# Optimization experiments

Hardware: AMD Instinct MI355X
Metric: run time of the kernel (lower is better)

The kernel has to match this reference:

```python
import jax, jax.numpy as jnp
import numpy as np

B, S, H, D, DM = 2, 512, 8, 32, 256  # batch, seq_len, n_head, d_k, d_model


def setup_inputs() -> dict:
    key = jax.random.key(0)
    ks = jax.random.split(key, 8)
    scale = 0.02
    return {
        "hidden_states": jax.random.normal(ks[0], (B, S, DM), dtype=jnp.float32),
        "rpe": jax.random.normal(ks[1], (B, S, S, D), dtype=jnp.float32),
        "w_q": jax.random.normal(ks[2], (DM, H * D), dtype=jnp.float32) * scale,
        "w_k": jax.random.normal(ks[3], (DM, H * D), dtype=jnp.float32) * scale,
        "w_v": jax.random.normal(ks[4], (DM, H * D), dtype=jnp.float32) * scale,
        "fc_w": jax.random.normal(ks[5], (H * D, DM), dtype=jnp.float32) * scale,
        "fc_b": jnp.zeros((DM,), dtype=jnp.float32),
        "ln_w": jnp.ones((DM,), dtype=jnp.float32),
        "ln_b": jnp.zeros((DM,), dtype=jnp.float32),
        "station_num": 256,
    }


def reference(hidden_states, rpe, w_q, w_k, w_v, fc_w, fc_b, ln_w, ln_b, station_num):
    b, s, dm = hidden_states.shape
    d = rpe.shape[-1]
    h = w_q.shape[1] // d

    def heads(x, w):
        # (b, s, dm) @ (dm, h*d) -> (b, h, s, d)
        return (x @ w).reshape(b, s, h, d).transpose(0, 2, 1, 3)

    q = heads(hidden_states, w_q)
    k = heads(hidden_states, w_k)
    v = heads(hidden_states, w_v)

    # torch: (q.unsqueeze(2) * k.unsqueeze(3) * rpe.unsqueeze(1)).sum(-1)
    # scores[b,h,i,j] = sum_d q[b,h,j,d] * k[b,h,i,d] * rpe[b,i,j,d]
    scores = jnp.einsum('bhjd,bhid,bijd->bhij', q, k, rpe) / jnp.sqrt(jnp.float32(d))

    # shielded mask: column j visible if j < station_num, plus the diagonal
    col = jnp.arange(s) < station_num                  # (s,)
    mask = col[None, :] | jnp.eye(s, dtype=bool)        # (s, s)
    scores = jnp.where(mask[None, None], scores, jnp.float32(-1e10))

    attn = jax.nn.softmax(scores, axis=-1)              # (b, h, s, s)
    out = jnp.einsum('bhij,bhjd->bhid', attn, v)        # (b, h, s, d)
    out = out.transpose(0, 2, 1, 3).reshape(b, s, h * d)

    ctx = out @ fc_w + fc_b + hidden_states             # residual
    mu = jnp.mean(ctx, axis=-1, keepdims=True)
    var = jnp.mean(jnp.square(ctx - mu), axis=-1, keepdims=True)
    ctx = (ctx - mu) / jnp.sqrt(var + 1e-6) * ln_w + ln_b
    return ctx
```

## Files before the change

### kernel.cpp

```cpp
#include <hip/hip_runtime.h>
#include <hip/hip_bf16.h>

#define B_  2
#define S_  512
#define H_  8
#define D_  32
#define DM_ 256
#define HD_ 256
#define NROW 4
#define TI  8
#define HC  2
#define NR  (TI * HC)
#define PSTR 520

__global__ __launch_bounds__(256) void qkv_kernel(
    const float* __restrict__ hid, const float* __restrict__ wq,
    const float* __restrict__ wk, const float* __restrict__ wv,
    float* __restrict__ qo, float* __restrict__ ko, float* __restrict__ vo)
{
  __shared__ float hs[NROW][DM_];
  const int r0 = blockIdx.x * NROW;
  const float* w   = (blockIdx.y == 0) ? wq : (blockIdx.y == 1) ? wk : wv;
  float*       out = (blockIdx.y == 0) ? qo : (blockIdx.y == 1) ? ko : vo;
  const int tid = threadIdx.x;

  for (int idx = tid; idx < NROW * DM_; idx += 256)
    hs[idx >> 8][idx & 255] = hid[r0 * DM_ + idx];
  __syncthreads();

  float acc[NROW] = {0.f, 0.f, 0.f, 0.f};
  const float* wp = w + tid;
  #pragma unroll 8
  for (int c4 = 0; c4 < DM_ / 4; ++c4) {
    const float w0 = wp[(4 * c4 + 0) * HD_];
    const float w1 = wp[(4 * c4 + 1) * HD_];
    const float w2 = wp[(4 * c4 + 2) * HD_];
    const float w3 = wp[(4 * c4 + 3) * HD_];
    #pragma unroll
    for (int r = 0; r < NROW; ++r) {
      const float4 hv = reinterpret_cast<const float4*>(&hs[r][0])[c4];
      acc[r] = fmaf(hv.x, w0, acc[r]);
      acc[r] = fmaf(hv.y, w1, acc[r]);
      acc[r] = fmaf(hv.z, w2, acc[r]);
      acc[r] = fmaf(hv.w, w3, acc[r]);
    }
  }
  const int h = tid >> 5, d = tid & 31;
  #pragma unroll
  for (int r = 0; r < NROW; ++r) {
    const int g = r0 + r;
    const int b = g >> 9, s = g & (S_ - 1);
    out[((b * H_ + h) * S_ + s) * D_ + d] = acc[r];
  }
}

__global__ __launch_bounds__(512, 2) void attn_kernel(
    const float* __restrict__ rpe, const float* __restrict__ q_ws,
    const float* __restrict__ k_ws, const float* __restrict__ v_ws,
    const int* __restrict__ station_p, float* __restrict__ o_ws)
{
  __shared__ float k_lds[NR * D_];
  __shared__ float p_lds[NR][PSTR];
  __shared__ float sums[NR];
  __shared__ float4 redv[8][NR][8];

  const int tid = threadIdx.x;
  const int n   = blockIdx.x;
  const int hg  = (n >> 3) & 3;
  const int t   = (n & 7) | ((n >> 5) << 3);
  const int b   = t >> 6;
  const int i0  = (t & 63) * TI;
  const int h0  = hg * HC;

  int station = station_p[0];
  if (station > S_) station = S_;
  if (station < 0)  station = 0;

  {
    const int r = tid >> 5, d = tid & 31;
    const int hh = r >> 3, ii = r & 7;
    k_lds[tid] = k_ws[((b * H_ + h0 + hh) * S_ + i0 + ii) * D_ + d];
  }
  __syncthreads();

  const int j = tid;
  const bool jlt = (j < station);
  const bool intile = (j >= i0) && (j < i0 + TI);

  float4 q0[8], q1[8];
  if (jlt || intile) {
    const float4* qp0 = reinterpret_cast<const float4*>(
        q_ws + ((b * H_ + h0 + 0) * S_ + j) * D_);
    const float4* qp1 = reinterpret_cast<const float4*>(
        q_ws + ((b * H_ + h0 + 1) * S_ + j) * D_);
    #pragma unroll
    for (int tt = 0; tt < 8; ++tt) { q0[tt] = qp0[tt]; q1[tt] = qp1[tt]; }
  }

  const float4* rbase = reinterpret_cast<const float4*>(
      rpe + (((size_t)b * S_ + i0) * S_ + j) * D_);
  const int rstride = S_ * D_ / 4;

  #pragma unroll
  for (int ii = 0; ii < TI; ++ii) {
    const int i = i0 + ii;
    const bool ok = jlt || (j == i);
    float s0 = -1e30f, s1 = -1e30f;
    if (ok) {
      const float4* rp  = rbase + ii * rstride;
      const float4* kp0 = reinterpret_cast<const float4*>(&k_lds[(0 * TI + ii) * D_]);
      const float4* kp1 = reinterpret_cast<const float4*>(&k_lds[(1 * TI + ii) * D_]);
      float a0 = 0.f, a1 = 0.f;
      #pragma unroll
      for (int tt = 0; tt < 8; ++tt) {
        const float4 rv = rp[tt];
        const float4 k0 = kp0[tt];
        const float4 k1 = kp1[tt];
        a0 = fmaf(q0[tt].x * k0.x, rv.x, a0);
        a0 = fmaf(q0[tt].y * k0.y, rv.y, a0);
        a0 = fmaf(q0[tt].z * k0.z, rv.z, a0);
        a0 = fmaf(q0[tt].w * k0.w, rv.w, a0);
        a1 = fmaf(q1[tt].x * k1.x, rv.x, a1);
        a1 = fmaf(q1[tt].y * k1.y, rv.y, a1);
        a1 = fmaf(q1[tt].z * k1.z, rv.z, a1);
        a1 = fmaf(q1[tt].w * k1.w, rv.w, a1);
      }
      s0 = a0 * 0.17677669529663687f;
      s1 = a1 * 0.17677669529663687f;
    }
    p_lds[0 * TI + ii][j] = s0;
    p_lds[1 * TI + ii][j] = s1;
  }
  __syncthreads();

  {
    const int w = tid >> 6, lane = tid & 63;
    for (int rr = w; rr < NR; rr += 8) {
      float m = -1e30f;
      #pragma unroll
      for (int jj = lane; jj < S_; jj += 64) m = fmaxf(m, p_lds[rr][jj]);
      #pragma unroll
      for (int o = 32; o; o >>= 1) m = fmaxf(m, __shfl_xor(m, o, 64));
      float sum = 0.f;
      #pragma unroll
      for (int jj = lane; jj < S_; jj += 64) {
        const float p = __expf(p_lds[rr][jj] - m);
        p_lds[rr][jj] = p;
        sum += p;
      }
      #pragma unroll
      for (int o = 32; o; o >>= 1) sum += __shfl_xor(sum, o, 64);
      if (lane == 0) sums[rr] = sum;
    }
  }
  __syncthreads();

  {
    const int part = tid >> 6;
    const int lane = tid & 63;
    const int ii = lane >> 3, d4 = lane & 7;
    const float4* vp0 = reinterpret_cast<const float4*>(
        v_ws + ((size_t)(b * H_ + h0 + 0) * S_) * D_) + d4;
    const float4* vp1 = reinterpret_cast<const float4*>(
        v_ws + ((size_t)(b * H_ + h0 + 1) * S_) * D_) + d4;
    float4 a0 = {0.f, 0.f, 0.f, 0.f};
    float4 a1 = {0.f, 0.f, 0.f, 0.f};
    #pragma unroll 4
    for (int jj = part; jj < station; jj += 8) {
      const float p0 = p_lds[0 * TI + ii][jj];
      const float p1 = p_lds[1 * TI + ii][jj];
      const float4 v0 = vp0[jj * (D_ / 4)];
      const float4 v1 = vp1[jj * (D_ / 4)];
      a0.x = fmaf(p0, v0.x, a0.x); a0.y = fmaf(p0, v0.y, a0.y);
      a0.z = fmaf(p0, v0.z, a0.z); a0.w = fmaf(p0, v0.w, a0.w);
      a1.x = fmaf(p1, v1.x, a1.x); a1.y = fmaf(p1, v1.y, a1.y);
      a1.z = fmaf(p1, v1.z, a1.z); a1.w = fmaf(p1, v1.w, a1.w);
    }
    const int ig = i0 + ii;
    if (ig >= station && part == (ig & 7)) {
      const float p0 = p_lds[0 * TI + ii][ig];
      const float p1 = p_lds[1 * TI + ii][ig];
      const float4 v0 = vp0[ig * (D_ / 4)];
      const float4 v1 = vp1[ig * (D_ / 4)];
      a0.x = fmaf(p0, v0.x, a0.x); a0.y = fmaf(p0, v0.y, a0.y);
      a0.z = fmaf(p0, v0.z, a0.z); a0.w = fmaf(p0, v0.w, a0.w);
      a1.x = fmaf(p1, v1.x, a1.x); a1.y = fmaf(p1, v1.y, a1.y);
      a1.z = fmaf(p1, v1.z, a1.z); a1.w = fmaf(p1, v1.w, a1.w);
    }
    redv[part][0 * TI + ii][d4] = a0;
    redv[part][1 * TI + ii][d4] = a1;
  }
  __syncthreads();
  if (tid < NR * 8) {
    const int r = tid >> 3, d4 = tid & 7;
    float4 a = redv[0][r][d4];
    #pragma unroll
    for (int p = 1; p < 8; ++p) {
      const float4 x = redv[p][r][d4];
      a.x += x.x; a.y += x.y; a.z += x.z; a.w += x.w;
    }
    const float inv = 1.f / sums[r];
    a.x *= inv; a.y *= inv; a.z *= inv; a.w *= inv;
    const int hh = r >> 3, ii = r & 7;
    reinterpret_cast<float4*>(
        o_ws + ((b * H_ + h0 + hh) * S_ + i0 + ii) * D_)[d4] = a;
  }
}

__global__ __launch_bounds__(256) void fc_ln_kernel(
    const float* __restrict__ o_ws, const float* __restrict__ fc_w,
    const float* __restrict__ fc_b, const float* __restrict__ hid,
    const float* __restrict__ ln_w, const float* __restrict__ ln_b,
    float* __restrict__ out)
{
  __shared__ float orow[NROW][HD_];
  __shared__ float red[NROW][4];
  const int tid = threadIdx.x;
  const int r0 = blockIdx.x * NROW;

  for (int idx = tid; idx < NROW * HD_; idx += 256) {
    const int r = idx >> 8, m = idx & 255;
    const int g = r0 + r;
    const int b = g >> 9, i = g & (S_ - 1);
    orow[r][m] = o_ws[((b * H_ + (m >> 5)) * S_ + i) * D_ + (m & 31)];
  }
  __syncthreads();

  float acc[NROW] = {0.f, 0.f, 0.f, 0.f};
  const float* wp = fc_w + tid;
  #pragma unroll 8
  for (int n4 = 0; n4 < HD_ / 4; ++n4) {
    const float w0 = wp[(4 * n4 + 0) * DM_];
    const float w1 = wp[(4 * n4 + 1) * DM_];
    const float w2 = wp[(4 * n4 + 2) * DM_];
    const float w3 = wp[(4 * n4 + 3) * DM_];
    #pragma unroll
    for (int r = 0; r < NROW; ++r) {
      const float4 ov = reinterpret_cast<const float4*>(&orow[r][0])[n4];
      acc[r] = fmaf(ov.x, w0, acc[r]);
      acc[r] = fmaf(ov.y, w1, acc[r]);
      acc[r] = fmaf(ov.z, w2, acc[r]);
      acc[r] = fmaf(ov.w, w3, acc[r]);
    }
  }
  const float bias = fc_b[tid];
  #pragma unroll
  for (int r = 0; r < NROW; ++r) acc[r] += bias + hid[(r0 + r) * DM_ + tid];

  const int w = tid >> 6, lane = tid & 63;
  float mu[NROW];
  #pragma unroll
  for (int r = 0; r < NROW; ++r) {
    float s = acc[r];
    #pragma unroll
    for (int o = 32; o; o >>= 1) s += __shfl_xor(s, o, 64);
    if (lane == 0) red[r][w] = s;
  }
  __syncthreads();
  #pragma unroll
  for (int r = 0; r < NROW; ++r)
    mu[r] = (red[r][0] + red[r][1] + red[r][2] + red[r][3]) * (1.f / DM_);
  __syncthreads();
  #pragma unroll
  for (int r = 0; r < NROW; ++r) {
    const float dd = acc[r] - mu[r];
    float s = dd * dd;
    #pragma unroll
    for (int o = 32; o; o >>= 1) s += __shfl_xor(s, o, 64);
    if (lane == 0) red[r][w] = s;
  }
  __syncthreads();
  const float lw = ln_w[tid], lb = ln_b[tid];
  #pragma unroll
  for (int r = 0; r < NROW; ++r) {
    const float var = (red[r][0] + red[r][1] + red[r][2] + red[r][3]) * (1.f / DM_);
    out[(r0 + r) * DM_ + tid] =
        (acc[r] - mu[r]) * rsqrtf(var + 1e-6f) * lw + lb;
  }
}

extern "C" void kernel_launch(void* const* d_in, const int* in_sizes, int n_in,
                              void* d_out, int out_size, void* d_ws, size_t ws_size,
                              hipStream_t stream) {
  const float* hid = (const float*)d_in[0];
  const float* rpe = (const float*)d_in[1];
  const float* wq  = (const float*)d_in[2];
  const float* wk  = (const float*)d_in[3];
  const float* wv  = (const float*)d_in[4];
  const float* fcw = (const float*)d_in[5];
  const float* fcb = (const float*)d_in[6];
  const float* lnw = (const float*)d_in[7];
  const float* lnb = (const float*)d_in[8];
  const int* station = (const int*)d_in[9];
  float* out = (float*)d_out;

  const size_t per = (size_t)B_ * H_ * S_ * D_;
  float* q_ws = (float*)d_ws;
  float* k_ws = q_ws + per;
  float* v_ws = k_ws + per;
  float* o_ws = v_ws + per;

  dim3 gA(B_ * S_ / NROW, 3);
  qkv_kernel<<<gA, 256, 0, stream>>>(hid, wq, wk, wv, q_ws, k_ws, v_ws);
  attn_kernel<<<B_ * (S_ / TI) * (H_ / HC), 512, 0, stream>>>(
      rpe, q_ws, k_ws, v_ws, station, o_ws);
  fc_ln_kernel<<<B_ * S_ / NROW, 256, 0, stream>>>(o_ws, fcw, fcb, hid, lnw, lnb, out);
}
```

Before: 168.4 us.

## Halve attention block size, loop over key halves, restrict softmax to visible columns

The attention kernel now runs 256 threads per block, and each thread handles two key columns. Each thread accumulates all 8 query rows per column in registers and reads K straight from global memory instead of staging it in LDS. The softmax only scans visible columns (j < station) plus the diagonal, instead of all 512 entries. The PV reduction splits across 4 partitions instead of 8. The aim is to cut wasted softmax work on masked columns and reuse q across rows. The cost is higher register pressure and less parallelism per block.

```diff
diff --git a/kernel.cpp b/kernel.cpp
--- a/kernel.cpp
+++ b/kernel.cpp
@@ -54,15 +54,14 @@
   }
 }
 
-__global__ __launch_bounds__(512, 2) void attn_kernel(
+__global__ __launch_bounds__(256, 3) void attn_kernel(
     const float* __restrict__ rpe, const float* __restrict__ q_ws,
     const float* __restrict__ k_ws, const float* __restrict__ v_ws,
     const int* __restrict__ station_p, float* __restrict__ o_ws)
 {
-  __shared__ float k_lds[NR * D_];
   __shared__ float p_lds[NR][PSTR];
   __shared__ float sums[NR];
-  __shared__ float4 redv[8][NR][8];
+  __shared__ float4 redv[4][NR][8];
 
   const int tid = threadIdx.x;
   const int n   = blockIdx.x;
@@ -73,84 +72,90 @@
   const int h0  = hg * HC;
 
   int station = station_p[0];
-  if (station > S_) station = S_;
-  if (station < 0)  station = 0;
-
-  {
-    const int r = tid >> 5, d = tid & 31;
-    const int hh = r >> 3, ii = r & 7;
-    k_lds[tid] = k_ws[((b * H_ + h0 + hh) * S_ + i0 + ii) * D_ + d];
-  }
-  __syncthreads();
-
-  const int j = tid;
-  const bool jlt = (j < station);
-  const bool intile = (j >= i0) && (j < i0 + TI);
-
-  float4 q0[8], q1[8];
-  if (jlt || intile) {
-    const float4* qp0 = reinterpret_cast<const float4*>(
-        q_ws + ((b * H_ + h0 + 0) * S_ + j) * D_);
-    const float4* qp1 = reinterpret_cast<const float4*>(
-        q_ws + ((b * H_ + h0 + 1) * S_ + j) * D_);
-    #pragma unroll
-    for (int tt = 0; tt < 8; ++tt) { q0[tt] = qp0[tt]; q1[tt] = qp1[tt]; }
-  }
-
-  const float4* rbase = reinterpret_cast<const float4*>(
-      rpe + (((size_t)b * S_ + i0) * S_ + j) * D_);
-  const int rstride = S_ * D_ / 4;
-
-  #pragma unroll
-  for (int ii = 0; ii < TI; ++ii) {
-    const int i = i0 + ii;
-    const bool ok = jlt || (j == i);
-    float s0 = -1e30f, s1 = -1e30f;
-    if (ok) {
-      const float4* rp  = rbase + ii * rstride;
-      const float4* kp0 = reinterpret_cast<const float4*>(&k_lds[(0 * TI + ii) * D_]);
-      const float4* kp1 = reinterpret_cast<const float4*>(&k_lds[(1 * TI + ii) * D_]);
-      float a0 = 0.f, a1 = 0.f;
+  station = station > S_ ? S_ : (station < 0 ? 0 : station);
+
+  const float* kb0 = k_ws + ((b * H_ + h0) * S_ + i0) * D_;
+  const float* kb1 = kb0 + S_ * D_;
+
+  #pragma unroll 1
+  for (int half = 0; half < 2; ++half) {
+    const int j  = tid + half * 256;
+    const int dt = j - i0;
+    const bool diag = ((unsigned)dt < (unsigned)TI);
+    if ((j < station) || diag) {
+      float a0[TI], a1[TI];
+      #pragma unroll
+      for (int ii = 0; ii < TI; ++ii) { a0[ii] = 0.f; a1[ii] = 0.f; }
+      const float* qp0 = q_ws + ((b * H_ + h0) * S_ + j) * D_;
+      const float* qp1 = qp0 + S_ * D_;
+      const float* rp  = rpe + (((size_t)b * S_ + i0) * S_ + j) * D_;
       #pragma unroll
       for (int tt = 0; tt < 8; ++tt) {
-        const float4 rv = rp[tt];
-        const float4 k0 = kp0[tt];
-        const float4 k1 = kp1[tt];
-        a0 = fmaf(q0[tt].x * k0.x, rv.x, a0);
-        a0 = fmaf(q0[tt].y * k0.y, rv.y, a0);
-        a0 = fmaf(q0[tt].z * k0.z, rv.z, a0);
-        a0 = fmaf(q0[tt].w * k0.w, rv.w, a0);
-        a1 = fmaf(q1[tt].x * k1.x, rv.x, a1);
-        a1 = fmaf(q1[tt].y * k1.y, rv.y, a1);
-        a1 = fmaf(q1[tt].z * k1.z, rv.z, a1);
-        a1 = fmaf(q1[tt].w * k1.w, rv.w, a1);
+        const float4 q0 = *reinterpret_cast<const float4*>(qp0 + tt * 4);
+        const float4 q1 = *reinterpret_cast<const float4*>(qp1 + tt * 4);
+        #pragma unroll
+        for (int ii = 0; ii < TI; ++ii) {
+          const float4 rv = *reinterpret_cast<const float4*>(rp + ii * (S_ * D_) + tt * 4);
+          const float4 k0 = *reinterpret_cast<const float4*>(kb0 + ii * D_ + tt * 4);
+          const float4 k1 = *reinterpret_cast<const float4*>(kb1 + ii * D_ + tt * 4);
+          a0[ii] = fmaf(q0.x * k0.x, rv.x, a0[ii]);
+          a0[ii] = fmaf(q0.y * k0.y, rv.y, a0[ii]);
+          a0[ii] = fmaf(q0.z * k0.z, rv.z, a0[ii]);
+          a0[ii] = fmaf(q0.w * k0.w, rv.w, a0[ii]);
+          a1[ii] = fmaf(q1.x * k1.x, rv.x, a1[ii]);
+          a1[ii] = fmaf(q1.y * k1.y, rv.y, a1[ii]);
+          a1[ii] = fmaf(q1.z * k1.z, rv.z, a1[ii]);
+          a1[ii] = fmaf(q1.w * k1.w, rv.w, a1[ii]);
+        }
       }
-      s0 = a0 * 0.17677669529663687f;
-      s1 = a1 * 0.17677669529663687f;
-    }
-    p_lds[0 * TI + ii][j] = s0;
-    p_lds[1 * TI + ii][j] = s1;
+      const float sc = 0.17677669529663687f;
+      if (j < station) {
+        #pragma unroll
+        for (int ii = 0; ii < TI; ++ii) {
+          p_lds[ii][j]      = a0[ii] * sc;
+          p_lds[TI + ii][j] = a1[ii] * sc;
+        }
+      } else {
+        #pragma unroll
+        for (int ii = 0; ii < TI; ++ii) {
+          if (dt == ii) {
+            p_lds[ii][j]      = a0[ii] * sc;
+            p_lds[TI + ii][j] = a1[ii] * sc;
+          }
+        }
+      }
+    }
   }
   __syncthreads();
 
   {
     const int w = tid >> 6, lane = tid & 63;
-    for (int rr = w; rr < NR; rr += 8) {
+    #pragma unroll
+    for (int k = 0; k < 4; ++k) {
+      const int r  = w * 4 + k;
+      const int ii = r & 7;
+      const int ig = i0 + ii;
+      const bool dx = (ig >= station);
       float m = -1e30f;
-      #pragma unroll
-      for (int jj = lane; jj < S_; jj += 64) m = fmaxf(m, p_lds[rr][jj]);
+      for (int jj = lane; jj < station; jj += 64) m = fmaxf(m, p_lds[r][jj]);
+      const float dv = dx ? p_lds[r][ig] : -1e30f;
+      m = fmaxf(m, dv);
       #pragma unroll
       for (int o = 32; o; o >>= 1) m = fmaxf(m, __shfl_xor(m, o, 64));
       float sum = 0.f;
-      #pragma unroll
-      for (int jj = lane; jj < S_; jj += 64) {
-        const float p = __expf(p_lds[rr][jj] - m);
-        p_lds[rr][jj] = p;
-        sum += p;
+      for (int jj = lane; jj < station; jj += 64) {
+        const float e = __expf(p_lds[r][jj] - m);
+        p_lds[r][jj] = e;
+        sum += e;
       }
       #pragma unroll
       for (int o = 32; o; o >>= 1) sum += __shfl_xor(sum, o, 64);
-      if (lane == 0) sums[rr] = sum;
+      if (dx) {
+        const float e = __expf(dv - m);
+        sum += e;
+        if (lane == 0) p_lds[r][ig] = e;
+      }
+      if (lane == 0) sums[r] = sum;
     }
   }
   __syncthreads();
@@ -159,43 +164,41 @@
     const int part = tid >> 6;
     const int lane = tid & 63;
     const int ii = lane >> 3, d4 = lane & 7;
-    const float4* vp0 = reinterpret_cast<const float4*>(
-        v_ws + ((size_t)(b * H_ + h0 + 0) * S_) * D_) + d4;
-    const float4* vp1 = reinterpret_cast<const float4*>(
-        v_ws + ((size_t)(b * H_ + h0 + 1) * S_) * D_) + d4;
+    const float* v0 = v_ws + (size_t)((b * H_ + h0) * S_) * D_;
+    const float* v1 = v0 + S_ * D_;
     float4 a0 = {0.f, 0.f, 0.f, 0.f};
     float4 a1 = {0.f, 0.f, 0.f, 0.f};
     #pragma unroll 4
-    for (int jj = part; jj < station; jj += 8) {
-      const float p0 = p_lds[0 * TI + ii][jj];
-      const float p1 = p_lds[1 * TI + ii][jj];
-      const float4 v0 = vp0[jj * (D_ / 4)];
-      const float4 v1 = vp1[jj * (D_ / 4)];
-      a0.x = fmaf(p0, v0.x, a0.x); a0.y = fmaf(p0, v0.y, a0.y);
-      a0.z = fmaf(p0, v0.z, a0.z); a0.w = fmaf(p0, v0.w, a0.w);
-      a1.x = fmaf(p1, v1.x, a1.x); a1.y = fmaf(p1, v1.y, a1.y);
-      a1.z = fmaf(p1, v1.z, a1.z); a1.w = fmaf(p1, v1.w, a1.w);
+    for (int jj = part; jj < station; jj += 4) {
+      const float p0 = p_lds[ii][jj];
+      const float p1 = p_lds[TI + ii][jj];
+      const float4 vv0 = *reinterpret_cast<const float4*>(v0 + jj * D_ + d4 * 4);
+      const float4 vv1 = *reinterpret_cast<const float4*>(v1 + jj * D_ + d4 * 4);
+      a0.x = fmaf(p0, vv0.x, a0.x); a0.y = fmaf(p0, vv0.y, a0.y);
+      a0.z = fmaf(p0, vv0.z, a0.z); a0.w = fmaf(p0, vv0.w, a0.w);
+      a1.x = fmaf(p1, vv1.x, a1.x); a1.y = fmaf(p1, vv1.y, a1.y);
+      a1.z = fmaf(p1, vv1.z, a1.z); a1.w = fmaf(p1, vv1.w, a1.w);
     }
     const int ig = i0 + ii;
-    if (ig >= station && part == (ig & 7)) {
-      const float p0 = p_lds[0 * TI + ii][ig];
-      const float p1 = p_lds[1 * TI + ii][ig];
-      const float4 v0 = vp0[ig * (D_ / 4)];
-      const float4 v1 = vp1[ig * (D_ / 4)];
-      a0.x = fmaf(p0, v0.x, a0.x); a0.y = fmaf(p0, v0.y, a0.y);
-      a0.z = fmaf(p0, v0.z, a0.z); a0.w = fmaf(p0, v0.w, a0.w);
-      a1.x = fmaf(p1, v1.x, a1.x); a1.y = fmaf(p1, v1.y, a1.y);
-      a1.z = fmaf(p1, v1.z, a1.z); a1.w = fmaf(p1, v1.w, a1.w);
-    }
-    redv[part][0 * TI + ii][d4] = a0;
-    redv[part][1 * TI + ii][d4] = a1;
+    if (ig >= station && part == (ig & 3)) {
+      const float p0 = p_lds[ii][ig];
+      const float p1 = p_lds[TI + ii][ig];
+      const float4 vv0 = *reinterpret_cast<const float4*>(v0 + ig * D_ + d4 * 4);
+      const float4 vv1 = *reinterpret_cast<const float4*>(v1 + ig * D_ + d4 * 4);
+      a0.x = fmaf(p0, vv0.x, a0.x); a0.y = fmaf(p0, vv0.y, a0.y);
+      a0.z = fmaf(p0, vv0.z, a0.z); a0.w = fmaf(p0, vv0.w, a0.w);
+      a1.x = fmaf(p1, vv1.x, a1.x); a1.y = fmaf(p1, vv1.y, a1.y);
+      a1.z = fmaf(p1, vv1.z, a1.z); a1.w = fmaf(p1, vv1.w, a1.w);
+    }
+    redv[part][ii][d4] = a0;
+    redv[part][TI + ii][d4] = a1;
   }
   __syncthreads();
   if (tid < NR * 8) {
     const int r = tid >> 3, d4 = tid & 7;
     float4 a = redv[0][r][d4];
     #pragma unroll
-    for (int p = 1; p < 8; ++p) {
+    for (int p = 1; p < 4; ++p) {
       const float4 x = redv[p][r][d4];
       a.x += x.x; a.y += x.y; a.z += x.z; a.w += x.w;
     }
@@ -302,7 +305,7 @@
 
   dim3 gA(B_ * S_ / NROW, 3);
   qkv_kernel<<<gA, 256, 0, stream>>>(hid, wq, wk, wv, q_ws, k_ws, v_ws);
-  attn_kernel<<<B_ * (S_ / TI) * (H_ / HC), 512, 0, stream>>>(
+  attn_kernel<<<B_ * (S_ / TI) * (H_ / HC), 256, 0, stream>>>(
       rpe, q_ws, k_ws, v_ws, station, o_ws);
   fc_ln_kernel<<<B_ * S_ / NROW, 256, 0, stream>>>(o_ws, fcw, fcb, hid, lnw, lnb, out);
 }
```

After: 191.2 us. 1.14x slower.
